# Performance work log

Measured on AMD Instinct MI355X. Metric: run time of the kernel, lower is better.

The kernel has to match this reference:

```python
import jax, jax.numpy as jnp
import numpy as np

EPS = 1e-5
K_SIZE, STRIDE, DILATION, N_HEADS = 8, 2, 2, 8


def ln2d(x, w, b):
    # LayerNorm2d: normalize over channel axis of NCHW
    m = x.mean(1, keepdims=True)
    v = x.var(1, keepdims=True)
    return (x - m) * jax.lax.rsqrt(v + EPS) * w[None, :, None, None] + b[None, :, None, None]


def setup_inputs() -> dict:
    key = jax.random.key(0)
    ks = jax.random.split(key, 8)
    B, C, H, W = 1, 64, 128, 128
    hid = 2 * C  # ffn_ratio = 2
    f = lambda k, s: jax.random.normal(k, s, jnp.float32) * 0.02
    return dict(
        x=jax.random.normal(ks[0], (B, C, H, W), jnp.float32),
        norm1_w=jnp.ones(C, jnp.float32), norm1_b=jnp.zeros(C, jnp.float32),
        qkv_w=f(ks[1], (3 * C, C)), qkv_b=jnp.zeros(3 * C, jnp.float32),
        qn_w=jnp.ones(C, jnp.float32), qn_b=jnp.zeros(C, jnp.float32),
        kn_w=jnp.ones(C, jnp.float32), kn_b=jnp.zeros(C, jnp.float32),
        proj_w=f(ks[2], (C, C)), proj_b=jnp.zeros(C, jnp.float32),
        gamma1=jnp.full((C,), 0.1, jnp.float32),
        norm2_w=jnp.ones(C, jnp.float32), norm2_b=jnp.zeros(C, jnp.float32),
        fc1_w=f(ks[3], (hid, C)), fc1_b=jnp.zeros(hid, jnp.float32),
        mn_w=jnp.ones(hid, jnp.float32), mn_b=jnp.zeros(hid, jnp.float32),
        fc2_w=f(ks[4], (C, hid)), fc2_b=jnp.zeros(C, jnp.float32),
        gamma2=jnp.full((C,), 0.1, jnp.float32),
    )


def reference(x, norm1_w, norm1_b, qkv_w, qkv_b, qn_w, qn_b, kn_w, kn_b,
              proj_w, proj_b, gamma1, norm2_w, norm2_b,
              fc1_w, fc1_b, mn_w, mn_b, fc2_w, fc2_b, gamma2):
    B, C, H, W = x.shape
    n = N_HEADS
    hd = C // n
    # strided + dilated neighborhood offsets (includes 0 at center)
    off = (jnp.arange(K_SIZE) * STRIDE - (K_SIZE * STRIDE) // 2) * DILATION

    # ---- neighborhood attention branch ----
    xn = ln2d(x, norm1_w, norm1_b)
    qkv = jnp.einsum('oc,bchw->bohw', qkv_w, xn) + qkv_b[None, :, None, None]
    q, k, v = jnp.split(qkv, 3, axis=1)
    q = ln2d(q, qn_w, qn_b)
    k = ln2d(k, kn_w, kn_b)
    q = q.reshape(B, n, hd, H, W)
    k = k.reshape(B, n, hd, H, W)
    v = v.reshape(B, n, hd, H, W)

    pos_h = jnp.arange(H)[:, None] + off[None, :]            # [H, k]
    vh = (pos_h >= 0) & (pos_h < H)
    ih = jnp.clip(pos_h, 0, H - 1)
    pos_w = jnp.arange(W)[:, None] + off[None, :]            # [W, k]
    vw = (pos_w >= 0) & (pos_w < W)
    iw = jnp.clip(pos_w, 0, W - 1)

    # gather neighborhoods: [B,n,hd,H,kh,W,kw]
    Kg = jnp.take(jnp.take(k, ih, axis=3), iw, axis=5)
    Vg = jnp.take(jnp.take(v, ih, axis=3), iw, axis=5)

    scores = jnp.einsum('bnchw,bnchiwj->bnhwij', q, Kg) * (hd ** -0.5)
    mask = vh[:, None, :, None] & vw[None, :, None, :]        # [H,W,kh,kw]
    scores = jnp.where(mask[None, None], scores, -jnp.inf)
    a = jax.nn.softmax(scores.reshape(B, n, H, W, -1), axis=-1).reshape(scores.shape)
    o = jnp.einsum('bnhwij,bnchiwj->bnchw', a, Vg).reshape(B, C, H, W)
    o = jnp.einsum('oc,bchw->bohw', proj_w, o) + proj_b[None, :, None, None]
    x = x + gamma1[None, :, None, None] * o                  # ls1 + residual (drop_path=0)

    # ---- ConvMlp branch: 1x1 conv -> norm -> silu -> 1x1 conv ----
    y = ln2d(x, norm2_w, norm2_b)
    h1 = jnp.einsum('oc,bchw->bohw', fc1_w, y) + fc1_b[None, :, None, None]
    h1 = jax.nn.silu(ln2d(h1, mn_w, mn_b))
    h2 = jnp.einsum('oc,bchw->bohw', fc2_w, h1) + fc2_b[None, :, None, None]
    return x + gamma2[None, :, None, None] * h2
```

## Files before the change

kernel.cpp:

```cpp
#include <hip/hip_runtime.h>
#include <math.h>

#define HW 16384
#define CC 64
#define HID 128
#define EPSV 1e-5f
#define ROW 36
#define QROW 205
#define HDSTR 131072


__global__ __launch_bounds__(256) void k_ln_qkv(
    const float* __restrict__ x,
    const float* __restrict__ n1w, const float* __restrict__ n1b,
    const float* __restrict__ qkvw, const float* __restrict__ qkvb,
    const float* __restrict__ qnw, const float* __restrict__ qnb,
    const float* __restrict__ knw, const float* __restrict__ knb,
    float* __restrict__ qo, float* __restrict__ ko, float* __restrict__ vo)
{
    __shared__ __align__(16) float xs[CC][ROW];
    __shared__ __align__(16) float qk[32][QROW];
    __shared__ __align__(16) float mu1[32], rs1[32], muq[32], rsq[32], muk[32], rsk[32];

    const int t = threadIdx.x;
    const int pix0 = blockIdx.x * 32;

    {
        const int c = t >> 2, pxq = (t & 3) * 8;
        *(float4*)&xs[c][pxq]     = *(const float4*)(x + c * HW + pix0 + pxq);
        *(float4*)&xs[c][pxq + 4] = *(const float4*)(x + c * HW + pix0 + pxq + 4);
    }
    __syncthreads();

    if (t < 128) {
        const int px = ((t >> 6) << 4) + (t & 15);
        const int part = (t & 63) >> 4;
        float s = 0.f, ss = 0.f;
        #pragma unroll
        for (int i = 0; i < 16; ++i) { float v = xs[part * 16 + i][px]; s += v; ss += v * v; }
        s += __shfl_xor(s, 16); ss += __shfl_xor(ss, 16);
        s += __shfl_xor(s, 32); ss += __shfl_xor(ss, 32);
        if (part == 0) {
            float m = s * (1.f / CC);
            mu1[px] = m;
            rs1[px] = rsqrtf(ss * (1.f / CC) - m * m + EPSV);
        }
    }
    __syncthreads();

    {
        const int c = t >> 2, pxq = (t & 3) * 8;
        const float wgt = n1w[c], bia = n1b[c];
        #pragma unroll
        for (int hh = 0; hh < 2; ++hh) {
            float4 v = *(float4*)&xs[c][pxq + hh * 4];
            float4 m4 = *(float4*)&mu1[pxq + hh * 4];
            float4 r4 = *(float4*)&rs1[pxq + hh * 4];
            v.x = (v.x - m4.x) * r4.x * wgt + bia;
            v.y = (v.y - m4.y) * r4.y * wgt + bia;
            v.z = (v.z - m4.z) * r4.z * wgt + bia;
            v.w = (v.w - m4.w) * r4.w * wgt + bia;
            *(float4*)&xs[c][pxq + hh * 4] = v;
        }
    }
    __syncthreads();

    {
        const int o0 = (t >> 3) * 6;
        const int px0 = (t & 7) * 4;
        float a[6][4];
        #pragma unroll
        for (int j = 0; j < 6; ++j) {
            float b = qkvb[o0 + j];
            a[j][0] = b; a[j][1] = b; a[j][2] = b; a[j][3] = b;
        }
        for (int c = 0; c < CC; c += 4) {
            float4 xv[4];
            #pragma unroll
            for (int i = 0; i < 4; ++i) xv[i] = *(float4*)&xs[c + i][px0];
            #pragma unroll
            for (int j = 0; j < 6; ++j) {
                float4 wv = *(const float4*)(qkvw + (o0 + j) * CC + c);
                #pragma unroll
                for (int pp = 0; pp < 4; ++pp) {
                    float xv0 = (&xv[0].x)[pp], xv1 = (&xv[1].x)[pp];
                    float xv2 = (&xv[2].x)[pp], xv3 = (&xv[3].x)[pp];
                    a[j][pp] += wv.x * xv0 + wv.y * xv1 + wv.z * xv2 + wv.w * xv3;
                }
            }
        }
        #pragma unroll
        for (int j = 0; j < 6; ++j) {
            #pragma unroll
            for (int pp = 0; pp < 4; ++pp) qk[px0 + pp][o0 + j] = a[j][pp];
        }
    }
    __syncthreads();

    if (t < 128) {
        const int px = ((t >> 6) << 4) + (t & 15);
        const int part = (t & 63) >> 4;
        float s = 0.f, ss = 0.f;
        #pragma unroll
        for (int i = 0; i < 16; ++i) { float v = qk[px][part * 16 + i]; s += v; ss += v * v; }
        s += __shfl_xor(s, 16); ss += __shfl_xor(ss, 16);
        s += __shfl_xor(s, 32); ss += __shfl_xor(ss, 32);
        if (part == 0) {
            float m = s * (1.f / CC);
            muq[px] = m;
            rsq[px] = rsqrtf(ss * (1.f / CC) - m * m + EPSV);
        }
    } else {
        const int t2 = t - 128;
        const int px = ((t2 >> 6) << 4) + (t2 & 15);
        const int part = (t2 & 63) >> 4;
        float s = 0.f, ss = 0.f;
        #pragma unroll
        for (int i = 0; i < 16; ++i) { float v = qk[px][CC + part * 16 + i]; s += v; ss += v * v; }
        s += __shfl_xor(s, 16); ss += __shfl_xor(ss, 16);
        s += __shfl_xor(s, 32); ss += __shfl_xor(ss, 32);
        if (part == 0) {
            float m = s * (1.f / CC);
            muk[px] = m;
            rsk[px] = rsqrtf(ss * (1.f / CC) - m * m + EPSV);
        }
    }
    __syncthreads();

    #pragma unroll
    for (int pass = 0; pass < 2; ++pass) {
        const int px = (t >> 4) + pass * 16;
        const int cg = t & 15;
        const int c = cg * 4;
        const int hd = cg >> 1;
        const int d4 = (cg & 1) * 4;
        const int pixel = pix0 + px;
        const int h = pixel >> 7, w = pixel & 127;
        const int pos = ((h >> 2) * 32 + (w >> 2)) * 16 + (h & 3) * 4 + (w & 3);
        const int gbase = hd * HDSTR + pos * 8 + d4;

        const float mq = muq[px], rq = rsq[px];
        float4 qv = *(float4*)&qk[px][c];
        float4 qw = *(const float4*)(qnw + c);
        float4 qb = *(const float4*)(qnb + c);
        qv.x = (qv.x - mq) * rq * qw.x + qb.x;
        qv.y = (qv.y - mq) * rq * qw.y + qb.y;
        qv.z = (qv.z - mq) * rq * qw.z + qb.z;
        qv.w = (qv.w - mq) * rq * qw.w + qb.w;
        *(float4*)(qo + gbase) = qv;

        const float mk = muk[px], rk = rsk[px];
        float4 kv = *(float4*)&qk[px][CC + c];
        float4 kw = *(const float4*)(knw + c);
        float4 kb = *(const float4*)(knb + c);
        kv.x = (kv.x - mk) * rk * kw.x + kb.x;
        kv.y = (kv.y - mk) * rk * kw.y + kb.y;
        kv.z = (kv.z - mk) * rk * kw.z + kb.z;
        kv.w = (kv.w - mk) * rk * kw.w + kb.w;
        *(float4*)(ko + gbase) = kv;

        float4 vv = *(float4*)&qk[px][2 * CC + c];
        *(float4*)(vo + gbase) = vv;
    }
}

__global__ __launch_bounds__(256) void k_attn(
    const float* __restrict__ q, const float* __restrict__ k, const float* __restrict__ v,
    float* __restrict__ o)
{
    __shared__ __align__(16) float kt[4][15][33][2];
    __shared__ __align__(16) float vt[4][15][33][2];

    const int t = threadIdx.x;
    const int band = blockIdx.x;
    const int sub  = blockIdx.y;
    const int head = blockIdx.z;
    const int hs0 = band * 8;

    const float* kb = k + head * HDSTR;
    const float* vb = v + head * HDSTR;

    for (int idx = t; idx < 960; idx += 256) {
        const int row = idx >> 6;
        const int rem = idx & 63;
        const int ws = rem >> 1;
        const int dh = rem & 1;
        int gr = hs0 - 4 + row;
        gr = gr < 0 ? 0 : (gr > 31 ? 31 : gr);
        const int gaddr = ((gr * 32 + ws) * 16 + sub) * 8 + dh * 4;
        const float4 kv4 = *(const float4*)(kb + gaddr);
        const float4 vv4 = *(const float4*)(vb + gaddr);
        const int dp = dh * 2;
        kt[dp][row][ws][0] = kv4.x;     kt[dp][row][ws][1] = kv4.y;
        kt[dp + 1][row][ws][0] = kv4.z; kt[dp + 1][row][ws][1] = kv4.w;
        vt[dp][row][ws][0] = vv4.x;     vt[dp][row][ws][1] = vv4.y;
        vt[dp + 1][row][ws][0] = vv4.z; vt[dp + 1][row][ws][1] = vv4.w;
    }

    const int r = t >> 5;
    const int ws = t & 31;
    const int hs = hs0 + r;

    const float* qp = q + head * HDSTR + ((hs * 32 + ws) * 16 + sub) * 8;
    const float4 q0 = *(const float4*)qp;
    const float4 q1 = *(const float4*)(qp + 4);
    const float scale = 0.35355339059327373f;

    __syncthreads();

    float s[64];
    float mx0 = -1e30f, mx1 = -1e30f, mx2 = -1e30f, mx3 = -1e30f;
    #pragma unroll
    for (int i = 0; i < 8; ++i) {
        const int lr = r + i;
        const bool vh = (unsigned)(hs + i - 4) < 32u;
        #pragma unroll
        for (int j = 0; j < 8; ++j) {
            const int cs = ws + j - 4;
            const bool valid = vh && ((unsigned)cs < 32u);
            const int cc = cs < 0 ? 0 : (cs > 31 ? 31 : cs);
            const float2 kA = *(const float2*)&kt[0][lr][cc][0];
            const float2 kB = *(const float2*)&kt[1][lr][cc][0];
            const float2 kC = *(const float2*)&kt[2][lr][cc][0];
            const float2 kD = *(const float2*)&kt[3][lr][cc][0];
            float sv = q0.x * kA.x + q0.y * kA.y + q0.z * kB.x + q0.w * kB.y
                     + q1.x * kC.x + q1.y * kC.y + q1.z * kD.x + q1.w * kD.y;
            sv *= scale;
            sv = valid ? sv : -INFINITY;
            s[i * 8 + j] = sv;
            if ((j & 3) == 0)      mx0 = fmaxf(mx0, sv);
            else if ((j & 3) == 1) mx1 = fmaxf(mx1, sv);
            else if ((j & 3) == 2) mx2 = fmaxf(mx2, sv);
            else                   mx3 = fmaxf(mx3, sv);
        }
    }
    const float mx = fmaxf(fmaxf(mx0, mx1), fmaxf(mx2, mx3));

    float l = 0.f;
    float a0 = 0.f, a1 = 0.f, a2 = 0.f, a3 = 0.f, a4 = 0.f, a5 = 0.f, a6 = 0.f, a7 = 0.f;
    #pragma unroll
    for (int i = 0; i < 8; ++i) {
        const int lr = r + i;
        #pragma unroll
        for (int j = 0; j < 8; ++j) {
            const int cs = ws + j - 4;
            const int cc = cs < 0 ? 0 : (cs > 31 ? 31 : cs);
            const float p = __expf(s[i * 8 + j] - mx);
            const float2 vA = *(const float2*)&vt[0][lr][cc][0];
            const float2 vB = *(const float2*)&vt[1][lr][cc][0];
            const float2 vC = *(const float2*)&vt[2][lr][cc][0];
            const float2 vD = *(const float2*)&vt[3][lr][cc][0];
            l += p;
            a0 += p * vA.x;  a1 += p * vA.y;
            a2 += p * vB.x;  a3 += p * vB.y;
            a4 += p * vC.x;  a5 += p * vC.y;
            a6 += p * vD.x;  a7 += p * vD.y;
        }
    }

    const float inv = 1.f / l;
    const int a = sub >> 2, b = sub & 3;
    const int h = hs * 4 + a, w = ws * 4 + b;
    float* op = o + (h * 128 + w) * 64 + head * 8;
    float4 r0 = {a0 * inv, a1 * inv, a2 * inv, a3 * inv};
    float4 r1 = {a4 * inv, a5 * inv, a6 * inv, a7 * inv};
    *(float4*)op = r0;
    *(float4*)(op + 4) = r1;
}

__global__ __launch_bounds__(256) void k_mlp(
    const float* __restrict__ x, const float* __restrict__ oatt,
    const float* __restrict__ pw, const float* __restrict__ pb,
    const float* __restrict__ g1,
    const float* __restrict__ n2w, const float* __restrict__ n2b,
    const float* __restrict__ f1w, const float* __restrict__ f1b,
    const float* __restrict__ mnw, const float* __restrict__ mnb,
    const float* __restrict__ f2w, const float* __restrict__ f2b,
    const float* __restrict__ g2,
    float* __restrict__ out)
{
    __shared__ __align__(16) float xres[CC][ROW];
    __shared__ __align__(16) float tb[CC][ROW];
    __shared__ __align__(16) float h1[HID][ROW];
    __shared__ __align__(16) float mu[32], rs[32];

    const int t = threadIdx.x;
    const int pix0 = blockIdx.x * 32;

    {
        const int c = t >> 2, pxq = (t & 3) * 8;
        *(float4*)&xres[c][pxq]     = *(const float4*)(x + c * HW + pix0 + pxq);
        *(float4*)&xres[c][pxq + 4] = *(const float4*)(x + c * HW + pix0 + pxq + 4);
    }
    #pragma unroll
    for (int pass = 0; pass < 2; ++pass) {
        const int px = (t >> 4) + pass * 16, cg = (t & 15) * 4;
        float4 ov = *(const float4*)(oatt + (pix0 + px) * CC + cg);
        tb[cg][px] = ov.x; tb[cg + 1][px] = ov.y; tb[cg + 2][px] = ov.z; tb[cg + 3][px] = ov.w;
    }
    __syncthreads();

    {
        const int o0 = (t >> 3) * 2;
        const int px0 = (t & 7) * 4;
        float a[2][4];
        #pragma unroll
        for (int j = 0; j < 2; ++j) {
            float b = pb[o0 + j];
            a[j][0] = b; a[j][1] = b; a[j][2] = b; a[j][3] = b;
        }
        for (int c = 0; c < CC; c += 4) {
            float4 xv[4];
            #pragma unroll
            for (int i = 0; i < 4; ++i) xv[i] = *(float4*)&tb[c + i][px0];
            #pragma unroll
            for (int j = 0; j < 2; ++j) {
                float4 wv = *(const float4*)(pw + (o0 + j) * CC + c);
                #pragma unroll
                for (int pp = 0; pp < 4; ++pp) {
                    a[j][pp] += wv.x * (&xv[0].x)[pp] + wv.y * (&xv[1].x)[pp]
                              + wv.z * (&xv[2].x)[pp] + wv.w * (&xv[3].x)[pp];
                }
            }
        }
        #pragma unroll
        for (int j = 0; j < 2; ++j) {
            const float gg = g1[o0 + j];
            #pragma unroll
            for (int pp = 0; pp < 4; ++pp) xres[o0 + j][px0 + pp] += gg * a[j][pp];
        }
    }
    __syncthreads();

    if (t < 128) {
        const int px = ((t >> 6) << 4) + (t & 15);
        const int part = (t & 63) >> 4;
        float s = 0.f, ss = 0.f;
        #pragma unroll
        for (int i = 0; i < 16; ++i) { float v = xres[part * 16 + i][px]; s += v; ss += v * v; }
        s += __shfl_xor(s, 16); ss += __shfl_xor(ss, 16);
        s += __shfl_xor(s, 32); ss += __shfl_xor(ss, 32);
        if (part == 0) {
            float m = s * (1.f / CC);
            mu[px] = m;
            rs[px] = rsqrtf(ss * (1.f / CC) - m * m + EPSV);
        }
    }
    __syncthreads();

    {
        const int c = t >> 2, pxq = (t & 3) * 8;
        const float wgt = n2w[c], bia = n2b[c];
        #pragma unroll
        for (int hh = 0; hh < 2; ++hh) {
            float4 v = *(float4*)&xres[c][pxq + hh * 4];
            float4 m4 = *(float4*)&mu[pxq + hh * 4];
            float4 r4 = *(float4*)&rs[pxq + hh * 4];
            v.x = (v.x - m4.x) * r4.x * wgt + bia;
            v.y = (v.y - m4.y) * r4.y * wgt + bia;
            v.z = (v.z - m4.z) * r4.z * wgt + bia;
            v.w = (v.w - m4.w) * r4.w * wgt + bia;
            *(float4*)&tb[c][pxq + hh * 4] = v;
        }
    }
    __syncthreads();

    {
        const int o0 = (t >> 3) * 4;
        const int px0 = (t & 7) * 4;
        float a[4][4];
        #pragma unroll
        for (int j = 0; j < 4; ++j) {
            float b = f1b[o0 + j];
            a[j][0] = b; a[j][1] = b; a[j][2] = b; a[j][3] = b;
        }
        for (int c = 0; c < CC; c += 4) {
            float4 xv[4];
            #pragma unroll
            for (int i = 0; i < 4; ++i) xv[i] = *(float4*)&tb[c + i][px0];
            #pragma unroll
            for (int j = 0; j < 4; ++j) {
                float4 wv = *(const float4*)(f1w + (o0 + j) * CC + c);
                #pragma unroll
                for (int pp = 0; pp < 4; ++pp) {
                    a[j][pp] += wv.x * (&xv[0].x)[pp] + wv.y * (&xv[1].x)[pp]
                              + wv.z * (&xv[2].x)[pp] + wv.w * (&xv[3].x)[pp];
                }
            }
        }
        #pragma unroll
        for (int j = 0; j < 4; ++j) {
            #pragma unroll
            for (int pp = 0; pp < 4; ++pp) h1[o0 + j][px0 + pp] = a[j][pp];
        }
    }
    __syncthreads();

    if (t < 128) {
        const int px = ((t >> 6) << 4) + (t & 15);
        const int part = (t & 63) >> 4;
        float s = 0.f, ss = 0.f;
        #pragma unroll
        for (int i = 0; i < 32; ++i) { float v = h1[part * 32 + i][px]; s += v; ss += v * v; }
        s += __shfl_xor(s, 16); ss += __shfl_xor(ss, 16);
        s += __shfl_xor(s, 32); ss += __shfl_xor(ss, 32);
        if (part == 0) {
            float m = s * (1.f / HID);
            mu[px] = m;
            rs[px] = rsqrtf(ss * (1.f / HID) - m * m + EPSV);
        }
    }
    __syncthreads();

    {
        const int c = t >> 1, ph = (t & 1) * 16;
        const float wgt = mnw[c], bia = mnb[c];
        #pragma unroll
        for (int qq = 0; qq < 4; ++qq) {
            float4 v = *(float4*)&h1[c][ph + qq * 4];
            float4 m4 = *(float4*)&mu[ph + qq * 4];
            float4 r4 = *(float4*)&rs[ph + qq * 4];
            float hv;
            hv = (v.x - m4.x) * r4.x * wgt + bia; v.x = hv / (1.f + __expf(-hv));
            hv = (v.y - m4.y) * r4.y * wgt + bia; v.y = hv / (1.f + __expf(-hv));
            hv = (v.z - m4.z) * r4.z * wgt + bia; v.z = hv / (1.f + __expf(-hv));
            hv = (v.w - m4.w) * r4.w * wgt + bia; v.w = hv / (1.f + __expf(-hv));
            *(float4*)&h1[c][ph + qq * 4] = v;
        }
    }
    __syncthreads();

    {
        const int o0 = (t >> 3) * 2;
        const int px0 = (t & 7) * 4;
        float a[2][4];
        #pragma unroll
        for (int j = 0; j < 2; ++j) {
            float b = f2b[o0 + j];
            a[j][0] = b; a[j][1] = b; a[j][2] = b; a[j][3] = b;
        }
        for (int c = 0; c < HID; c += 4) {
            float4 xv[4];
            #pragma unroll
            for (int i = 0; i < 4; ++i) xv[i] = *(float4*)&h1[c + i][px0];
            #pragma unroll
            for (int j = 0; j < 2; ++j) {
                float4 wv = *(const float4*)(f2w + (o0 + j) * HID + c);
                #pragma unroll
                for (int pp = 0; pp < 4; ++pp) {
                    a[j][pp] += wv.x * (&xv[0].x)[pp] + wv.y * (&xv[1].x)[pp]
                              + wv.z * (&xv[2].x)[pp] + wv.w * (&xv[3].x)[pp];
                }
            }
        }
        #pragma unroll
        for (int j = 0; j < 2; ++j) {
            const float gg = g2[o0 + j];
            float4 xr = *(float4*)&xres[o0 + j][px0];
            float4 ov = {xr.x + gg * a[j][0], xr.y + gg * a[j][1],
                         xr.z + gg * a[j][2], xr.w + gg * a[j][3]};
            *(float4*)(out + (o0 + j) * HW + pix0 + px0) = ov;
        }
    }
}

extern "C" void kernel_launch(void* const* d_in, const int* in_sizes, int n_in,
                              void* d_out, int out_size, void* d_ws, size_t ws_size,
                              hipStream_t stream) {
    (void)in_sizes; (void)n_in; (void)out_size; (void)ws_size;
    const float* x      = (const float*)d_in[0];
    const float* n1w    = (const float*)d_in[1];
    const float* n1b    = (const float*)d_in[2];
    const float* qkvw   = (const float*)d_in[3];
    const float* qkvb   = (const float*)d_in[4];
    const float* qnw    = (const float*)d_in[5];
    const float* qnb    = (const float*)d_in[6];
    const float* knw    = (const float*)d_in[7];
    const float* knb    = (const float*)d_in[8];
    const float* pw     = (const float*)d_in[9];
    const float* pb     = (const float*)d_in[10];
    const float* g1     = (const float*)d_in[11];
    const float* n2w    = (const float*)d_in[12];
    const float* n2b    = (const float*)d_in[13];
    const float* f1w    = (const float*)d_in[14];
    const float* f1b    = (const float*)d_in[15];
    const float* mnw    = (const float*)d_in[16];
    const float* mnb    = (const float*)d_in[17];
    const float* f2w    = (const float*)d_in[18];
    const float* f2b    = (const float*)d_in[19];
    const float* g2     = (const float*)d_in[20];
    float* out = (float*)d_out;

    float* ws = (float*)d_ws;
    const size_t CHW = (size_t)CC * HW;
    float* qo   = ws;
    float* ko   = ws + CHW;
    float* vo   = ws + 2 * CHW;
    float* oatt = ws + 3 * CHW;

    k_ln_qkv<<<dim3(HW / 32), dim3(256), 0, stream>>>(
        x, n1w, n1b, qkvw, qkvb, qnw, qnb, knw, knb, qo, ko, vo);
    k_attn<<<dim3(4, 16, 8), dim3(256), 0, stream>>>(qo, ko, vo, oatt);
    k_mlp<<<dim3(HW / 32), dim3(256), 0, stream>>>(
        x, oatt, pw, pb, g1, n2w, n2b, f1w, f1b, mnw, mnb, f2w, f2b, g2, out);
}
```

Baseline: 145.5 us.

## Fuse three kernels into one persistent kernel with grid barriers

Merges the LN+QKV, neighborhood attention and MLP kernels into a single 512-block kernel whose phases share a union of shared-memory layouts and are separated by software grid barriers (atomic counter plus spin). The aim is to remove the launch gaps and tail effects between the three dependent kernels. In exchange it adds a memset launch and spin-wait barrier costs, and it relies on all 512 blocks being co-resident (launch_bounds 256,2); if they are not, the kernel deadlocks. The attention phase must now map onto 512 blocks instead of its original 4x16x8 grid.

```diff
diff --git a/kernel.cpp b/kernel.cpp
--- a/kernel.cpp
+++ b/kernel.cpp
@@ -8,268 +8,51 @@
 #define ROW 36
 #define QROW 205
 #define HDSTR 131072
-
-
-__global__ __launch_bounds__(256) void k_ln_qkv(
+#define NBLK 512
+
+
+struct SA {
+    float xs[CC][ROW];
+    float qk[32][QROW];
+    float mu1[32], rs1[32], muq[32], rsq[32], muk[32], rsk[32];
+};
+struct SB {
+    float kt[4][15][33][2];
+    float vt[4][15][33][2];
+};
+struct SC {
+    float xres[CC][ROW];
+    float tb[CC][ROW];
+    float h1[HID][ROW];
+    float mu[32], rs[32];
+};
+union SU {
+    SA a;
+    SB b;
+    SC c;
+};
+
+__device__ __forceinline__ void grid_barrier(unsigned* bar, unsigned target) {
+    __syncthreads();
+    if (threadIdx.x == 0) {
+        __threadfence();
+        atomicAdd(bar, 1u);
+        unsigned v;
+        do {
+            __builtin_amdgcn_s_sleep(2);
+            v = __hip_atomic_load(bar, __ATOMIC_RELAXED, __HIP_MEMORY_SCOPE_AGENT);
+        } while (v < target);
+        __threadfence();
+    }
+    __syncthreads();
+}
+
+__global__ __launch_bounds__(256, 2) void k_fused(
     const float* __restrict__ x,
     const float* __restrict__ n1w, const float* __restrict__ n1b,
     const float* __restrict__ qkvw, const float* __restrict__ qkvb,
     const float* __restrict__ qnw, const float* __restrict__ qnb,
     const float* __restrict__ knw, const float* __restrict__ knb,
-    float* __restrict__ qo, float* __restrict__ ko, float* __restrict__ vo)
-{
-    __shared__ __align__(16) float xs[CC][ROW];
-    __shared__ __align__(16) float qk[32][QROW];
-    __shared__ __align__(16) float mu1[32], rs1[32], muq[32], rsq[32], muk[32], rsk[32];
-
-    const int t = threadIdx.x;
-    const int pix0 = blockIdx.x * 32;
-
-    {
-        const int c = t >> 2, pxq = (t & 3) * 8;
-        *(float4*)&xs[c][pxq]     = *(const float4*)(x + c * HW + pix0 + pxq);
-        *(float4*)&xs[c][pxq + 4] = *(const float4*)(x + c * HW + pix0 + pxq + 4);
-    }
-    __syncthreads();
-
-    if (t < 128) {
-        const int px = ((t >> 6) << 4) + (t & 15);
-        const int part = (t & 63) >> 4;
-        float s = 0.f, ss = 0.f;
-        #pragma unroll
-        for (int i = 0; i < 16; ++i) { float v = xs[part * 16 + i][px]; s += v; ss += v * v; }
-        s += __shfl_xor(s, 16); ss += __shfl_xor(ss, 16);
-        s += __shfl_xor(s, 32); ss += __shfl_xor(ss, 32);
-        if (part == 0) {
-            float m = s * (1.f / CC);
-            mu1[px] = m;
-            rs1[px] = rsqrtf(ss * (1.f / CC) - m * m + EPSV);
-        }
-    }
-    __syncthreads();
-
-    {
-        const int c = t >> 2, pxq = (t & 3) * 8;
-        const float wgt = n1w[c], bia = n1b[c];
-        #pragma unroll
-        for (int hh = 0; hh < 2; ++hh) {
-            float4 v = *(float4*)&xs[c][pxq + hh * 4];
-            float4 m4 = *(float4*)&mu1[pxq + hh * 4];
-            float4 r4 = *(float4*)&rs1[pxq + hh * 4];
-            v.x = (v.x - m4.x) * r4.x * wgt + bia;
-            v.y = (v.y - m4.y) * r4.y * wgt + bia;
-            v.z = (v.z - m4.z) * r4.z * wgt + bia;
-            v.w = (v.w - m4.w) * r4.w * wgt + bia;
-            *(float4*)&xs[c][pxq + hh * 4] = v;
-        }
-    }
-    __syncthreads();
-
-    {
-        const int o0 = (t >> 3) * 6;
-        const int px0 = (t & 7) * 4;
-        float a[6][4];
-        #pragma unroll
-        for (int j = 0; j < 6; ++j) {
-            float b = qkvb[o0 + j];
-            a[j][0] = b; a[j][1] = b; a[j][2] = b; a[j][3] = b;
-        }
-        for (int c = 0; c < CC; c += 4) {
-            float4 xv[4];
-            #pragma unroll
-            for (int i = 0; i < 4; ++i) xv[i] = *(float4*)&xs[c + i][px0];
-            #pragma unroll
-            for (int j = 0; j < 6; ++j) {
-                float4 wv = *(const float4*)(qkvw + (o0 + j) * CC + c);
-                #pragma unroll
-                for (int pp = 0; pp < 4; ++pp) {
-                    float xv0 = (&xv[0].x)[pp], xv1 = (&xv[1].x)[pp];
-                    float xv2 = (&xv[2].x)[pp], xv3 = (&xv[3].x)[pp];
-                    a[j][pp] += wv.x * xv0 + wv.y * xv1 + wv.z * xv2 + wv.w * xv3;
-                }
-            }
-        }
-        #pragma unroll
-        for (int j = 0; j < 6; ++j) {
-            #pragma unroll
-            for (int pp = 0; pp < 4; ++pp) qk[px0 + pp][o0 + j] = a[j][pp];
-        }
-    }
-    __syncthreads();
-
-    if (t < 128) {
-        const int px = ((t >> 6) << 4) + (t & 15);
-        const int part = (t & 63) >> 4;
-        float s = 0.f, ss = 0.f;
-        #pragma unroll
-        for (int i = 0; i < 16; ++i) { float v = qk[px][part * 16 + i]; s += v; ss += v * v; }
-        s += __shfl_xor(s, 16); ss += __shfl_xor(ss, 16);
-        s += __shfl_xor(s, 32); ss += __shfl_xor(ss, 32);
-        if (part == 0) {
-            float m = s * (1.f / CC);
-            muq[px] = m;
-            rsq[px] = rsqrtf(ss * (1.f / CC) - m * m + EPSV);
-        }
-    } else {
-        const int t2 = t - 128;
-        const int px = ((t2 >> 6) << 4) + (t2 & 15);
-        const int part = (t2 & 63) >> 4;
-        float s = 0.f, ss = 0.f;
-        #pragma unroll
-        for (int i = 0; i < 16; ++i) { float v = qk[px][CC + part * 16 + i]; s += v; ss += v * v; }
-        s += __shfl_xor(s, 16); ss += __shfl_xor(ss, 16);
-        s += __shfl_xor(s, 32); ss += __shfl_xor(ss, 32);
-        if (part == 0) {
-            float m = s * (1.f / CC);
-            muk[px] = m;
-            rsk[px] = rsqrtf(ss * (1.f / CC) - m * m + EPSV);
-        }
-    }
-    __syncthreads();
-
-    #pragma unroll
-    for (int pass = 0; pass < 2; ++pass) {
-        const int px = (t >> 4) + pass * 16;
-        const int cg = t & 15;
-        const int c = cg * 4;
-        const int hd = cg >> 1;
-        const int d4 = (cg & 1) * 4;
-        const int pixel = pix0 + px;
-        const int h = pixel >> 7, w = pixel & 127;
-        const int pos = ((h >> 2) * 32 + (w >> 2)) * 16 + (h & 3) * 4 + (w & 3);
-        const int gbase = hd * HDSTR + pos * 8 + d4;
-
-        const float mq = muq[px], rq = rsq[px];
-        float4 qv = *(float4*)&qk[px][c];
-        float4 qw = *(const float4*)(qnw + c);
-        float4 qb = *(const float4*)(qnb + c);
-        qv.x = (qv.x - mq) * rq * qw.x + qb.x;
-        qv.y = (qv.y - mq) * rq * qw.y + qb.y;
-        qv.z = (qv.z - mq) * rq * qw.z + qb.z;
-        qv.w = (qv.w - mq) * rq * qw.w + qb.w;
-        *(float4*)(qo + gbase) = qv;
-
-        const float mk = muk[px], rk = rsk[px];
-        float4 kv = *(float4*)&qk[px][CC + c];
-        float4 kw = *(const float4*)(knw + c);
-        float4 kb = *(const float4*)(knb + c);
-        kv.x = (kv.x - mk) * rk * kw.x + kb.x;
-        kv.y = (kv.y - mk) * rk * kw.y + kb.y;
-        kv.z = (kv.z - mk) * rk * kw.z + kb.z;
-        kv.w = (kv.w - mk) * rk * kw.w + kb.w;
-        *(float4*)(ko + gbase) = kv;
-
-        float4 vv = *(float4*)&qk[px][2 * CC + c];
-        *(float4*)(vo + gbase) = vv;
-    }
-}
-
-__global__ __launch_bounds__(256) void k_attn(
-    const float* __restrict__ q, const float* __restrict__ k, const float* __restrict__ v,
-    float* __restrict__ o)
-{
-    __shared__ __align__(16) float kt[4][15][33][2];
-    __shared__ __align__(16) float vt[4][15][33][2];
-
-    const int t = threadIdx.x;
-    const int band = blockIdx.x;
-    const int sub  = blockIdx.y;
-    const int head = blockIdx.z;
-    const int hs0 = band * 8;
-
-    const float* kb = k + head * HDSTR;
-    const float* vb = v + head * HDSTR;
-
-    for (int idx = t; idx < 960; idx += 256) {
-        const int row = idx >> 6;
-        const int rem = idx & 63;
-        const int ws = rem >> 1;
-        const int dh = rem & 1;
-        int gr = hs0 - 4 + row;
-        gr = gr < 0 ? 0 : (gr > 31 ? 31 : gr);
-        const int gaddr = ((gr * 32 + ws) * 16 + sub) * 8 + dh * 4;
-        const float4 kv4 = *(const float4*)(kb + gaddr);
-        const float4 vv4 = *(const float4*)(vb + gaddr);
-        const int dp = dh * 2;
-        kt[dp][row][ws][0] = kv4.x;     kt[dp][row][ws][1] = kv4.y;
-        kt[dp + 1][row][ws][0] = kv4.z; kt[dp + 1][row][ws][1] = kv4.w;
-        vt[dp][row][ws][0] = vv4.x;     vt[dp][row][ws][1] = vv4.y;
-        vt[dp + 1][row][ws][0] = vv4.z; vt[dp + 1][row][ws][1] = vv4.w;
-    }
-
-    const int r = t >> 5;
-    const int ws = t & 31;
-    const int hs = hs0 + r;
-
-    const float* qp = q + head * HDSTR + ((hs * 32 + ws) * 16 + sub) * 8;
-    const float4 q0 = *(const float4*)qp;
-    const float4 q1 = *(const float4*)(qp + 4);
-    const float scale = 0.35355339059327373f;
-
-    __syncthreads();
-
-    float s[64];
-    float mx0 = -1e30f, mx1 = -1e30f, mx2 = -1e30f, mx3 = -1e30f;
-    #pragma unroll
-    for (int i = 0; i < 8; ++i) {
-        const int lr = r + i;
-        const bool vh = (unsigned)(hs + i - 4) < 32u;
-        #pragma unroll
-        for (int j = 0; j < 8; ++j) {
-            const int cs = ws + j - 4;
-            const bool valid = vh && ((unsigned)cs < 32u);
-            const int cc = cs < 0 ? 0 : (cs > 31 ? 31 : cs);
-            const float2 kA = *(const float2*)&kt[0][lr][cc][0];
-            const float2 kB = *(const float2*)&kt[1][lr][cc][0];
-            const float2 kC = *(const float2*)&kt[2][lr][cc][0];
-            const float2 kD = *(const float2*)&kt[3][lr][cc][0];
-            float sv = q0.x * kA.x + q0.y * kA.y + q0.z * kB.x + q0.w * kB.y
-                     + q1.x * kC.x + q1.y * kC.y + q1.z * kD.x + q1.w * kD.y;
-            sv *= scale;
-            sv = valid ? sv : -INFINITY;
-            s[i * 8 + j] = sv;
-            if ((j & 3) == 0)      mx0 = fmaxf(mx0, sv);
-            else if ((j & 3) == 1) mx1 = fmaxf(mx1, sv);
-            else if ((j & 3) == 2) mx2 = fmaxf(mx2, sv);
-            else                   mx3 = fmaxf(mx3, sv);
-        }
-    }
-    const float mx = fmaxf(fmaxf(mx0, mx1), fmaxf(mx2, mx3));
-
-    float l = 0.f;
-    float a0 = 0.f, a1 = 0.f, a2 = 0.f, a3 = 0.f, a4 = 0.f, a5 = 0.f, a6 = 0.f, a7 = 0.f;
-    #pragma unroll
-    for (int i = 0; i < 8; ++i) {
-        const int lr = r + i;
-        #pragma unroll
-        for (int j = 0; j < 8; ++j) {
-            const int cs = ws + j - 4;
-            const int cc = cs < 0 ? 0 : (cs > 31 ? 31 : cs);
-            const float p = __expf(s[i * 8 + j] - mx);
-            const float2 vA = *(const float2*)&vt[0][lr][cc][0];
-            const float2 vB = *(const float2*)&vt[1][lr][cc][0];
-            const float2 vC = *(const float2*)&vt[2][lr][cc][0];
-            const float2 vD = *(const float2*)&vt[3][lr][cc][0];
-            l += p;
-            a0 += p * vA.x;  a1 += p * vA.y;
-            a2 += p * vB.x;  a3 += p * vB.y;
-            a4 += p * vC.x;  a5 += p * vC.y;
-            a6 += p * vD.x;  a7 += p * vD.y;
-        }
-    }
-
-    const float inv = 1.f / l;
-    const int a = sub >> 2, b = sub & 3;
-    const int h = hs * 4 + a, w = ws * 4 + b;
-    float* op = o + (h * 128 + w) * 64 + head * 8;
-    float4 r0 = {a0 * inv, a1 * inv, a2 * inv, a3 * inv};
-    float4 r1 = {a4 * inv, a5 * inv, a6 * inv, a7 * inv};
-    *(float4*)op = r0;
-    *(float4*)(op + 4) = r1;
-}
-
-__global__ __launch_bounds__(256) void k_mlp(
-    const float* __restrict__ x, const float* __restrict__ oatt,
     const float* __restrict__ pw, const float* __restrict__ pb,
     const float* __restrict__ g1,
     const float* __restrict__ n2w, const float* __restrict__ n2b,
@@ -277,189 +60,442 @@
     const float* __restrict__ mnw, const float* __restrict__ mnb,
     const float* __restrict__ f2w, const float* __restrict__ f2b,
     const float* __restrict__ g2,
-    float* __restrict__ out)
+    float* __restrict__ qo, float* __restrict__ ko, float* __restrict__ vo,
+    float* __restrict__ oatt,
+    float* __restrict__ out,
+    unsigned* bar)
 {
-    __shared__ __align__(16) float xres[CC][ROW];
-    __shared__ __align__(16) float tb[CC][ROW];
-    __shared__ __align__(16) float h1[HID][ROW];
-    __shared__ __align__(16) float mu[32], rs[32];
-
+    __shared__ __align__(16) SU sm;
     const int t = threadIdx.x;
-    const int pix0 = blockIdx.x * 32;
+    const int bid = blockIdx.x;
 
     {
-        const int c = t >> 2, pxq = (t & 3) * 8;
-        *(float4*)&xres[c][pxq]     = *(const float4*)(x + c * HW + pix0 + pxq);
-        *(float4*)&xres[c][pxq + 4] = *(const float4*)(x + c * HW + pix0 + pxq + 4);
+        const int pix0 = bid * 32;
+        auto& xs = sm.a.xs;
+        auto& qk = sm.a.qk;
+
+        {
+            const int c = t >> 2, pxq = (t & 3) * 8;
+            *(float4*)&xs[c][pxq]     = *(const float4*)(x + c * HW + pix0 + pxq);
+            *(float4*)&xs[c][pxq + 4] = *(const float4*)(x + c * HW + pix0 + pxq + 4);
+        }
+        __syncthreads();
+
+        if (t < 128) {
+            const int px = ((t >> 6) << 4) + (t & 15);
+            const int part = (t & 63) >> 4;
+            float s = 0.f, ss = 0.f;
+            #pragma unroll
+            for (int i = 0; i < 16; ++i) { float v = xs[part * 16 + i][px]; s += v; ss += v * v; }
+            s += __shfl_xor(s, 16); ss += __shfl_xor(ss, 16);
+            s += __shfl_xor(s, 32); ss += __shfl_xor(ss, 32);
+            if (part == 0) {
+                float m = s * (1.f / CC);
+                sm.a.mu1[px] = m;
+                sm.a.rs1[px] = rsqrtf(ss * (1.f / CC) - m * m + EPSV);
+            }
+        }
+        __syncthreads();
+
+        {
+            const int c = t >> 2, pxq = (t & 3) * 8;
+            const float wgt = n1w[c], bia = n1b[c];
+            #pragma unroll
+            for (int hh = 0; hh < 2; ++hh) {
+                float4 v = *(float4*)&xs[c][pxq + hh * 4];
+                float4 m4 = *(float4*)&sm.a.mu1[pxq + hh * 4];
+                float4 r4 = *(float4*)&sm.a.rs1[pxq + hh * 4];
+                v.x = (v.x - m4.x) * r4.x * wgt + bia;
+                v.y = (v.y - m4.y) * r4.y * wgt + bia;
+                v.z = (v.z - m4.z) * r4.z * wgt + bia;
+                v.w = (v.w - m4.w) * r4.w * wgt + bia;
+                *(float4*)&xs[c][pxq + hh * 4] = v;
+            }
+        }
+        __syncthreads();
+
+        {
+            const int o0 = (t >> 3) * 6;
+            const int px0 = (t & 7) * 4;
+            float a[6][4];
+            #pragma unroll
+            for (int j = 0; j < 6; ++j) {
+                float b = qkvb[o0 + j];
+                a[j][0] = b; a[j][1] = b; a[j][2] = b; a[j][3] = b;
+            }
+            for (int c = 0; c < CC; c += 4) {
+                float4 xv[4];
+                #pragma unroll
+                for (int i = 0; i < 4; ++i) xv[i] = *(float4*)&xs[c + i][px0];
+                #pragma unroll
+                for (int j = 0; j < 6; ++j) {
+                    float4 wv = *(const float4*)(qkvw + (o0 + j) * CC + c);
+                    #pragma unroll
+                    for (int pp = 0; pp < 4; ++pp) {
+                        a[j][pp] += wv.x * (&xv[0].x)[pp] + wv.y * (&xv[1].x)[pp]
+                                  + wv.z * (&xv[2].x)[pp] + wv.w * (&xv[3].x)[pp];
+                    }
+                }
+            }
+            #pragma unroll
+            for (int j = 0; j < 6; ++j) {
+                #pragma unroll
+                for (int pp = 0; pp < 4; ++pp) qk[px0 + pp][o0 + j] = a[j][pp];
+            }
+        }
+        __syncthreads();
+
+        if (t < 128) {
+            const int px = ((t >> 6) << 4) + (t & 15);
+            const int part = (t & 63) >> 4;
+            float s = 0.f, ss = 0.f;
+            #pragma unroll
+            for (int i = 0; i < 16; ++i) { float v = qk[px][part * 16 + i]; s += v; ss += v * v; }
+            s += __shfl_xor(s, 16); ss += __shfl_xor(ss, 16);
+            s += __shfl_xor(s, 32); ss += __shfl_xor(ss, 32);
+            if (part == 0) {
+                float m = s * (1.f / CC);
+                sm.a.muq[px] = m;
+                sm.a.rsq[px] = rsqrtf(ss * (1.f / CC) - m * m + EPSV);
+            }
+        } else {
+            const int t2 = t - 128;
+            const int px = ((t2 >> 6) << 4) + (t2 & 15);
+            const int part = (t2 & 63) >> 4;
+            float s = 0.f, ss = 0.f;
+            #pragma unroll
+            for (int i = 0; i < 16; ++i) { float v = qk[px][CC + part * 16 + i]; s += v; ss += v * v; }
+            s += __shfl_xor(s, 16); ss += __shfl_xor(ss, 16);
+            s += __shfl_xor(s, 32); ss += __shfl_xor(ss, 32);
+            if (part == 0) {
+                float m = s * (1.f / CC);
+                sm.a.muk[px] = m;
+                sm.a.rsk[px] = rsqrtf(ss * (1.f / CC) - m * m + EPSV);
+            }
+        }
+        __syncthreads();
+
+        #pragma unroll
+        for (int pass = 0; pass < 2; ++pass) {
+            const int px = (t >> 4) + pass * 16;
+            const int cg2 = t & 15;
+            const int c = cg2 * 4;
+            const int hd = cg2 >> 1;
+            const int d4 = (cg2 & 1) * 4;
+            const int pixel = pix0 + px;
+            const int h = pixel >> 7, w = pixel & 127;
+            const int pos = ((h >> 2) * 32 + (w >> 2)) * 16 + (h & 3) * 4 + (w & 3);
+            const int gbase = hd * HDSTR + pos * 8 + d4;
+
+            const float mq = sm.a.muq[px], rq = sm.a.rsq[px];
+            float4 qv = *(float4*)&qk[px][c];
+            float4 qw = *(const float4*)(qnw + c);
+            float4 qb = *(const float4*)(qnb + c);
+            qv.x = (qv.x - mq) * rq * qw.x + qb.x;
+            qv.y = (qv.y - mq) * rq * qw.y + qb.y;
+            qv.z = (qv.z - mq) * rq * qw.z + qb.z;
+            qv.w = (qv.w - mq) * rq * qw.w + qb.w;
+            *(float4*)(qo + gbase) = qv;
+
+            const float mk = sm.a.muk[px], rk = sm.a.rsk[px];
+            float4 kv = *(float4*)&qk[px][CC + c];
+            float4 kw = *(const float4*)(knw + c);
+            float4 kb = *(const float4*)(knb + c);
+            kv.x = (kv.x - mk) * rk * kw.x + kb.x;
+            kv.y = (kv.y - mk) * rk * kw.y + kb.y;
+            kv.z = (kv.z - mk) * rk * kw.z + kb.z;
+            kv.w = (kv.w - mk) * rk * kw.w + kb.w;
+            *(float4*)(ko + gbase) = kv;
+
+            float4 vv = *(float4*)&qk[px][2 * CC + c];
+            *(float4*)(vo + gbase) = vv;
+        }
     }
-    #pragma unroll
-    for (int pass = 0; pass < 2; ++pass) {
-        const int px = (t >> 4) + pass * 16, cg = (t & 15) * 4;
-        float4 ov = *(const float4*)(oatt + (pix0 + px) * CC + cg);
-        tb[cg][px] = ov.x; tb[cg + 1][px] = ov.y; tb[cg + 2][px] = ov.z; tb[cg + 3][px] = ov.w;
+
+    grid_barrier(bar, NBLK);
+
+    {
+        const int band = bid & 3;
+        const int sub  = (bid >> 2) & 15;
+        const int head = bid >> 6;
+        const int hs0 = band * 8;
+
+        auto& kt = sm.b.kt;
+        auto& vt = sm.b.vt;
+
+        const float* kb = ko + head * HDSTR;
+        const float* vb = vo + head * HDSTR;
+
+        for (int idx = t; idx < 960; idx += 256) {
+            const int row = idx >> 6;
+            const int rem = idx & 63;
+            const int wsc = rem >> 1;
+            const int dh = rem & 1;
+            int gr = hs0 - 4 + row;
+            gr = gr < 0 ? 0 : (gr > 31 ? 31 : gr);
+            const int gaddr = ((gr * 32 + wsc) * 16 + sub) * 8 + dh * 4;
+            const float4 kv4 = *(const float4*)(kb + gaddr);
+            const float4 vv4 = *(const float4*)(vb + gaddr);
+            const int dp = dh * 2;
+            kt[dp][row][wsc][0] = kv4.x;     kt[dp][row][wsc][1] = kv4.y;
+            kt[dp + 1][row][wsc][0] = kv4.z; kt[dp + 1][row][wsc][1] = kv4.w;
+            vt[dp][row][wsc][0] = vv4.x;     vt[dp][row][wsc][1] = vv4.y;
+            vt[dp + 1][row][wsc][0] = vv4.z; vt[dp + 1][row][wsc][1] = vv4.w;
+        }
+
+        const int r = t >> 5;
+        const int wsc = t & 31;
+        const int hs = hs0 + r;
+
+        const float* qp = qo + head * HDSTR + ((hs * 32 + wsc) * 16 + sub) * 8;
+        const float4 q0 = *(const float4*)qp;
+        const float4 q1 = *(const float4*)(qp + 4);
+        const float scale = 0.35355339059327373f;
+
+        __syncthreads();
+
+        float s[64];
+        float mx0 = -1e30f, mx1 = -1e30f, mx2 = -1e30f, mx3 = -1e30f;
+        #pragma unroll
+        for (int i = 0; i < 8; ++i) {
+            const int lr = r + i;
+            const bool vh = (unsigned)(hs + i - 4) < 32u;
+            #pragma unroll
+            for (int j = 0; j < 8; ++j) {
+                const int cs = wsc + j - 4;
+                const bool valid = vh && ((unsigned)cs < 32u);
+                const int cc = cs < 0 ? 0 : (cs > 31 ? 31 : cs);
+                const float2 kA = *(const float2*)&kt[0][lr][cc][0];
+                const float2 kB = *(const float2*)&kt[1][lr][cc][0];
+                const float2 kC = *(const float2*)&kt[2][lr][cc][0];
+                const float2 kD = *(const float2*)&kt[3][lr][cc][0];
+                float sv = q0.x * kA.x + q0.y * kA.y + q0.z * kB.x + q0.w * kB.y
+                         + q1.x * kC.x + q1.y * kC.y + q1.z * kD.x + q1.w * kD.y;
+                sv *= scale;
+                sv = valid ? sv : -INFINITY;
+                s[i * 8 + j] = sv;
+                if ((j & 3) == 0)      mx0 = fmaxf(mx0, sv);
+                else if ((j & 3) == 1) mx1 = fmaxf(mx1, sv);
+                else if ((j & 3) == 2) mx2 = fmaxf(mx2, sv);
+                else                   mx3 = fmaxf(mx3, sv);
+            }
+        }
+        const float mx = fmaxf(fmaxf(mx0, mx1), fmaxf(mx2, mx3));
+
+        float l = 0.f;
+        float a0 = 0.f, a1 = 0.f, a2 = 0.f, a3 = 0.f, a4 = 0.f, a5 = 0.f, a6 = 0.f, a7 = 0.f;
+        #pragma unroll
+        for (int i = 0; i < 8; ++i) {
+            const int lr = r + i;
+            #pragma unroll
+            for (int j = 0; j < 8; ++j) {
+                const int cs = wsc + j - 4;
+                const int cc = cs < 0 ? 0 : (cs > 31 ? 31 : cs);
+                const float p = __expf(s[i * 8 + j] - mx);
+                const float2 vA = *(const float2*)&vt[0][lr][cc][0];
+                const float2 vB = *(const float2*)&vt[1][lr][cc][0];
+                const float2 vC = *(const float2*)&vt[2][lr][cc][0];
+                const float2 vD = *(const float2*)&vt[3][lr][cc][0];
+                l += p;
+                a0 += p * vA.x;  a1 += p * vA.y;
+                a2 += p * vB.x;  a3 += p * vB.y;
+                a4 += p * vC.x;  a5 += p * vC.y;
+                a6 += p * vD.x;  a7 += p * vD.y;
+            }
+        }
+
+        const float inv = 1.f / l;
+        const int a = sub >> 2, b = sub & 3;
+        const int h = hs * 4 + a, w = wsc * 4 + b;
+        float* op = oatt + (h * 128 + w) * 64 + head * 8;
+        float4 r0 = {a0 * inv, a1 * inv, a2 * inv, a3 * inv};
+        float4 r1 = {a4 * inv, a5 * inv, a6 * inv, a7 * inv};
+        *(float4*)op = r0;
+        *(float4*)(op + 4) = r1;
     }
-    __syncthreads();
+
+    grid_barrier(bar, 2 * NBLK);
 
     {
-        const int o0 = (t >> 3) * 2;
-        const int px0 = (t & 7) * 4;
-        float a[2][4];
+        const int pix0 = bid * 32;
+        auto& xres = sm.c.xres;
+        auto& tb = sm.c.tb;
+        auto& h1 = sm.c.h1;
+
+        {
+            const int c = t >> 2, pxq = (t & 3) * 8;
+            *(float4*)&xres[c][pxq]     = *(const float4*)(x + c * HW + pix0 + pxq);
+            *(float4*)&xres[c][pxq + 4] = *(const float4*)(x + c * HW + pix0 + pxq + 4);
+        }
         #pragma unroll
-        for (int j = 0; j < 2; ++j) {
-            float b = pb[o0 + j];
-            a[j][0] = b; a[j][1] = b; a[j][2] = b; a[j][3] = b;
-        }
-        for (int c = 0; c < CC; c += 4) {
-            float4 xv[4];
-            #pragma unroll
-            for (int i = 0; i < 4; ++i) xv[i] = *(float4*)&tb[c + i][px0];
+        for (int pass = 0; pass < 2; ++pass) {
+            const int px = (t >> 4) + pass * 16, cg2 = (t & 15) * 4;
+            float4 ov = *(const float4*)(oatt + (pix0 + px) * CC + cg2);
+            tb[cg2][px] = ov.x; tb[cg2 + 1][px] = ov.y; tb[cg2 + 2][px] = ov.z; tb[cg2 + 3][px] = ov.w;
+        }
+        __syncthreads();
+
+        {
+            const int o0 = (t >> 3) * 2;
+            const int px0 = (t & 7) * 4;
+            float a[2][4];
             #pragma unroll
             for (int j = 0; j < 2; ++j) {
-                float4 wv = *(const float4*)(pw + (o0 + j) * CC + c);
-                #pragma unroll
-                for (int pp = 0; pp < 4; ++pp) {
-                    a[j][pp] += wv.x * (&xv[0].x)[pp] + wv.y * (&xv[1].x)[pp]
-                              + wv.z * (&xv[2].x)[pp] + wv.w * (&xv[3].x)[pp];
+                float b = pb[o0 + j];
+                a[j][0] = b; a[j][1] = b; a[j][2] = b; a[j][3] = b;
+            }
+            for (int c = 0; c < CC; c += 4) {
+                float4 xv[4];
+                #pragma unroll
+                for (int i = 0; i < 4; ++i) xv[i] = *(float4*)&tb[c + i][px0];
+                #pragma unroll
+                for (int j = 0; j < 2; ++j) {
+                    float4 wv = *(const float4*)(pw + (o0 + j) * CC + c);
+                    #pragma unroll
+                    for (int pp = 0; pp < 4; ++pp) {
+                        a[j][pp] += wv.x * (&xv[0].x)[pp] + wv.y * (&xv[1].x)[pp]
+                                  + wv.z * (&xv[2].x)[pp] + wv.w * (&xv[3].x)[pp];
+                    }
                 }
             }
-        }
-        #pragma unroll
-        for (int j = 0; j < 2; ++j) {
-            const float gg = g1[o0 + j];
-            #pragma unroll
-            for (int pp = 0; pp < 4; ++pp) xres[o0 + j][px0 + pp] += gg * a[j][pp];
-        }
-    }
-    __syncthreads();
-
-    if (t < 128) {
-        const int px = ((t >> 6) << 4) + (t & 15);
-        const int part = (t & 63) >> 4;
-        float s = 0.f, ss = 0.f;
-        #pragma unroll
-        for (int i = 0; i < 16; ++i) { float v = xres[part * 16 + i][px]; s += v; ss += v * v; }
-        s += __shfl_xor(s, 16); ss += __shfl_xor(ss, 16);
-        s += __shfl_xor(s, 32); ss += __shfl_xor(ss, 32);
-        if (part == 0) {
-            float m = s * (1.f / CC);
-            mu[px] = m;
-            rs[px] = rsqrtf(ss * (1.f / CC) - m * m + EPSV);
-        }
-    }
-    __syncthreads();
-
-    {
-        const int c = t >> 2, pxq = (t & 3) * 8;
-        const float wgt = n2w[c], bia = n2b[c];
-        #pragma unroll
-        for (int hh = 0; hh < 2; ++hh) {
-            float4 v = *(float4*)&xres[c][pxq + hh * 4];
-            float4 m4 = *(float4*)&mu[pxq + hh * 4];
-            float4 r4 = *(float4*)&rs[pxq + hh * 4];
-            v.x = (v.x - m4.x) * r4.x * wgt + bia;
-            v.y = (v.y - m4.y) * r4.y * wgt + bia;
-            v.z = (v.z - m4.z) * r4.z * wgt + bia;
-            v.w = (v.w - m4.w) * r4.w * wgt + bia;
-            *(float4*)&tb[c][pxq + hh * 4] = v;
-        }
-    }
-    __syncthreads();
-
-    {
-        const int o0 = (t >> 3) * 4;
-        const int px0 = (t & 7) * 4;
-        float a[4][4];
-        #pragma unroll
-        for (int j = 0; j < 4; ++j) {
-            float b = f1b[o0 + j];
-            a[j][0] = b; a[j][1] = b; a[j][2] = b; a[j][3] = b;
-        }
-        for (int c = 0; c < CC; c += 4) {
-            float4 xv[4];
-            #pragma unroll
-            for (int i = 0; i < 4; ++i) xv[i] = *(float4*)&tb[c + i][px0];
+            #pragma unroll
+            for (int j = 0; j < 2; ++j) {
+                const float gg = g1[o0 + j];
+                #pragma unroll
+                for (int pp = 0; pp < 4; ++pp) xres[o0 + j][px0 + pp] += gg * a[j][pp];
+            }
+        }
+        __syncthreads();
+
+        if (t < 128) {
+            const int px = ((t >> 6) << 4) + (t & 15);
+            const int part = (t & 63) >> 4;
+            float s = 0.f, ss = 0.f;
+            #pragma unroll
+            for (int i = 0; i < 16; ++i) { float v = xres[part * 16 + i][px]; s += v; ss += v * v; }
+            s += __shfl_xor(s, 16); ss += __shfl_xor(ss, 16);
+            s += __shfl_xor(s, 32); ss += __shfl_xor(ss, 32);
+            if (part == 0) {
+                float m = s * (1.f / CC);
+                sm.c.mu[px] = m;
+                sm.c.rs[px] = rsqrtf(ss * (1.f / CC) - m * m + EPSV);
+            }
+        }
+        __syncthreads();
+
+        {
+            const int c = t >> 2, pxq = (t & 3) * 8;
+            const float wgt = n2w[c], bia = n2b[c];
+            #pragma unroll
+            for (int hh = 0; hh < 2; ++hh) {
+                float4 v = *(float4*)&xres[c][pxq + hh * 4];
+                float4 m4 = *(float4*)&sm.c.mu[pxq + hh * 4];
+                float4 r4 = *(float4*)&sm.c.rs[pxq + hh * 4];
+                v.x = (v.x - m4.x) * r4.x * wgt + bia;
+                v.y = (v.y - m4.y) * r4.y * wgt + bia;
+                v.z = (v.z - m4.z) * r4.z * wgt + bia;
+                v.w = (v.w - m4.w) * r4.w * wgt + bia;
+                *(float4*)&tb[c][pxq + hh * 4] = v;
+            }
+        }
+        __syncthreads();
+
+        {
+            const int o0 = (t >> 3) * 4;
+            const int px0 = (t & 7) * 4;
+            float a[4][4];
             #pragma unroll
             for (int j = 0; j < 4; ++j) {
-                float4 wv = *(const float4*)(f1w + (o0 + j) * CC + c);
-                #pragma unroll
-                for (int pp = 0; pp < 4; ++pp) {
-                    a[j][pp] += wv.x * (&xv[0].x)[pp] + wv.y * (&xv[1].x)[pp]
-                              + wv.z * (&xv[2].x)[pp] + wv.w * (&xv[3].x)[pp];
+                float b = f1b[o0 + j];
+                a[j][0] = b; a[j][1] = b; a[j][2] = b; a[j][3] = b;
+            }
+            for (int c = 0; c < CC; c += 4) {
+                float4 xv[4];
+                #pragma unroll
+                for (int i = 0; i < 4; ++i) xv[i] = *(float4*)&tb[c + i][px0];
+                #pragma unroll
+                for (int j = 0; j < 4; ++j) {
+                    float4 wv = *(const float4*)(f1w + (o0 + j) * CC + c);
+                    #pragma unroll
+                    for (int pp = 0; pp < 4; ++pp) {
+                        a[j][pp] += wv.x * (&xv[0].x)[pp] + wv.y * (&xv[1].x)[pp]
+                                  + wv.z * (&xv[2].x)[pp] + wv.w * (&xv[3].x)[pp];
+                    }
                 }
             }
-        }
-        #pragma unroll
-        for (int j = 0; j < 4; ++j) {
-            #pragma unroll
-            for (int pp = 0; pp < 4; ++pp) h1[o0 + j][px0 + pp] = a[j][pp];
-        }
-    }
-    __syncthreads();
-
-    if (t < 128) {
-        const int px = ((t >> 6) << 4) + (t & 15);
-        const int part = (t & 63) >> 4;
-        float s = 0.f, ss = 0.f;
-        #pragma unroll
-        for (int i = 0; i < 32; ++i) { float v = h1[part * 32 + i][px]; s += v; ss += v * v; }
-        s += __shfl_xor(s, 16); ss += __shfl_xor(ss, 16);
-        s += __shfl_xor(s, 32); ss += __shfl_xor(ss, 32);
-        if (part == 0) {
-            float m = s * (1.f / HID);
-            mu[px] = m;
-            rs[px] = rsqrtf(ss * (1.f / HID) - m * m + EPSV);
-        }
-    }
-    __syncthreads();
-
-    {
-        const int c = t >> 1, ph = (t & 1) * 16;
-        const float wgt = mnw[c], bia = mnb[c];
-        #pragma unroll
-        for (int qq = 0; qq < 4; ++qq) {
-            float4 v = *(float4*)&h1[c][ph + qq * 4];
-            float4 m4 = *(float4*)&mu[ph + qq * 4];
-            float4 r4 = *(float4*)&rs[ph + qq * 4];
-            float hv;
-            hv = (v.x - m4.x) * r4.x * wgt + bia; v.x = hv / (1.f + __expf(-hv));
-            hv = (v.y - m4.y) * r4.y * wgt + bia; v.y = hv / (1.f + __expf(-hv));
-            hv = (v.z - m4.z) * r4.z * wgt + bia; v.z = hv / (1.f + __expf(-hv));
-            hv = (v.w - m4.w) * r4.w * wgt + bia; v.w = hv / (1.f + __expf(-hv));
-            *(float4*)&h1[c][ph + qq * 4] = v;
-        }
-    }
-    __syncthreads();
-
-    {
-        const int o0 = (t >> 3) * 2;
-        const int px0 = (t & 7) * 4;
-        float a[2][4];
-        #pragma unroll
-        for (int j = 0; j < 2; ++j) {
-            float b = f2b[o0 + j];
-            a[j][0] = b; a[j][1] = b; a[j][2] = b; a[j][3] = b;
-        }
-        for (int c = 0; c < HID; c += 4) {
-            float4 xv[4];
-            #pragma unroll
-            for (int i = 0; i < 4; ++i) xv[i] = *(float4*)&h1[c + i][px0];
+            #pragma unroll
+            for (int j = 0; j < 4; ++j) {
+                #pragma unroll
+                for (int pp = 0; pp < 4; ++pp) h1[o0 + j][px0 + pp] = a[j][pp];
+            }
+        }
+        __syncthreads();
+
+        if (t < 128) {
+            const int px = ((t >> 6) << 4) + (t & 15);
+            const int part = (t & 63) >> 4;
+            float s = 0.f, ss = 0.f;
+            #pragma unroll
+            for (int i = 0; i < 32; ++i) { float v = h1[part * 32 + i][px]; s += v; ss += v * v; }
+            s += __shfl_xor(s, 16); ss += __shfl_xor(ss, 16);
+            s += __shfl_xor(s, 32); ss += __shfl_xor(ss, 32);
+            if (part == 0) {
+                float m = s * (1.f / HID);
+                sm.c.mu[px] = m;
+                sm.c.rs[px] = rsqrtf(ss * (1.f / HID) - m * m + EPSV);
+            }
+        }
+        __syncthreads();
+
+        {
+            const int c = t >> 1, ph = (t & 1) * 16;
+            const float wgt = mnw[c], bia = mnb[c];
+            #pragma unroll
+            for (int qq = 0; qq < 4; ++qq) {
+                float4 v = *(float4*)&h1[c][ph + qq * 4];
+                float4 m4 = *(float4*)&sm.c.mu[ph + qq * 4];
+                float4 r4 = *(float4*)&sm.c.rs[ph + qq * 4];
+                float hv;
+                hv = (v.x - m4.x) * r4.x * wgt + bia; v.x = hv / (1.f + __expf(-hv));
+                hv = (v.y - m4.y) * r4.y * wgt + bia; v.y = hv / (1.f + __expf(-hv));
+                hv = (v.z - m4.z) * r4.z * wgt + bia; v.z = hv / (1.f + __expf(-hv));
+                hv = (v.w - m4.w) * r4.w * wgt + bia; v.w = hv / (1.f + __expf(-hv));
+                *(float4*)&h1[c][ph + qq * 4] = v;
+            }
+        }
+        __syncthreads();
+
+        {
+            const int o0 = (t >> 3) * 2;
+            const int px0 = (t & 7) * 4;
+            float a[2][4];
             #pragma unroll
             for (int j = 0; j < 2; ++j) {
-                float4 wv = *(const float4*)(f2w + (o0 + j) * HID + c);
-                #pragma unroll
-                for (int pp = 0; pp < 4; ++pp) {
-                    a[j][pp] += wv.x * (&xv[0].x)[pp] + wv.y * (&xv[1].x)[pp]
-                              + wv.z * (&xv[2].x)[pp] + wv.w * (&xv[3].x)[pp];
+                float b = f2b[o0 + j];
+                a[j][0] = b; a[j][1] = b; a[j][2] = b; a[j][3] = b;
+            }
+            for (int c = 0; c < HID; c += 4) {
+                float4 xv[4];
+                #pragma unroll
+                for (int i = 0; i < 4; ++i) xv[i] = *(float4*)&h1[c + i][px0];
+                #pragma unroll
+                for (int j = 0; j < 2; ++j) {
+                    float4 wv = *(const float4*)(f2w + (o0 + j) * HID + c);
+                    #pragma unroll
+                    for (int pp = 0; pp < 4; ++pp) {
+                        a[j][pp] += wv.x * (&xv[0].x)[pp] + wv.y * (&xv[1].x)[pp]
+                                  + wv.z * (&xv[2].x)[pp] + wv.w * (&xv[3].x)[pp];
+                    }
                 }
             }
-        }
-        #pragma unroll
-        for (int j = 0; j < 2; ++j) {
-            const float gg = g2[o0 + j];
-            float4 xr = *(float4*)&xres[o0 + j][px0];
-            float4 ov = {xr.x + gg * a[j][0], xr.y + gg * a[j][1],
-                         xr.z + gg * a[j][2], xr.w + gg * a[j][3]};
-            *(float4*)(out + (o0 + j) * HW + pix0 + px0) = ov;
+            #pragma unroll
+            for (int j = 0; j < 2; ++j) {
+                const float gg = g2[o0 + j];
+                float4 xr = *(float4*)&xres[o0 + j][px0];
+                float4 ov = {xr.x + gg * a[j][0], xr.y + gg * a[j][1],
+                             xr.z + gg * a[j][2], xr.w + gg * a[j][3]};
+                *(float4*)(out + (o0 + j) * HW + pix0 + px0) = ov;
+            }
         }
     }
 }
@@ -497,10 +533,12 @@
     float* ko   = ws + CHW;
     float* vo   = ws + 2 * CHW;
     float* oatt = ws + 3 * CHW;
-
-    k_ln_qkv<<<dim3(HW / 32), dim3(256), 0, stream>>>(
-        x, n1w, n1b, qkvw, qkvb, qnw, qnb, knw, knb, qo, ko, vo);
-    k_attn<<<dim3(4, 16, 8), dim3(256), 0, stream>>>(qo, ko, vo, oatt);
-    k_mlp<<<dim3(HW / 32), dim3(256), 0, stream>>>(
-        x, oatt, pw, pb, g1, n2w, n2b, f1w, f1b, mnw, mnb, f2w, f2b, g2, out);
+    unsigned* bar = (unsigned*)(ws + 4 * CHW);
+
+    hipMemsetAsync((void*)bar, 0, 64, stream);
+
+    k_fused<<<dim3(NBLK), dim3(256), 0, stream>>>(
+        x, n1w, n1b, qkvw, qkvb, qnw, qnb, knw, knb,
+        pw, pb, g1, n2w, n2b, f1w, f1b, mnw, mnb, f2w, f2b, g2,
+        qo, ko, vo, oatt, out, bar);
 }
```

Result: slower. 254.7 us (+75.1%).
